# Kernel tuning notes

Measured on AMD Instinct MI355X. Metric: run time of the kernel, lower is better.

The kernel has to match this reference:

```python
import jax, jax.numpy as jnp
import numpy as np

LN_EPS = 1e-5

def layer_norm(h, gamma, beta):
    mu = jnp.mean(h, axis=-1, keepdims=True)
    var = jnp.mean(jnp.square(h - mu), axis=-1, keepdims=True)
    return (h - mu) * jax.lax.rsqrt(var + LN_EPS) * gamma + beta

def gcn_conv(x, src, dst, W, b, n_nodes):
    # PyG GCNConv: h = X W; out = D^-1/2 (A + I) D^-1/2 h + b
    h = x @ W
    deg = jax.ops.segment_sum(jnp.ones_like(src, dtype=h.dtype), dst, num_segments=n_nodes)
    dinv = jax.lax.rsqrt(jnp.maximum(deg, 1.0))  # deg >= 1 due to self-loops
    norm = dinv[src] * dinv[dst]                  # [E]
    msg = h[src] * norm[:, None]                  # [E, d]
    return jax.ops.segment_sum(msg, dst, num_segments=n_nodes) + b

def setup_inputs() -> dict:
    key = jax.random.key(0)
    ks = jax.random.split(key, 8)
    N, E, Cin, Ch, Cout = 10000, 160000, 256, 512, 256
    x = jax.random.normal(ks[0], (N, Cin), dtype=jnp.float32)
    edge_index = jax.random.randint(ks[1], (2, E), 0, N, dtype=jnp.int64)
    W1 = jax.random.normal(ks[2], (Cin, Ch), dtype=jnp.float32) * (1.0 / np.sqrt(Cin))
    b1 = jnp.zeros((Ch,), dtype=jnp.float32)
    gamma1 = jnp.ones((Ch,), dtype=jnp.float32)
    beta1 = jnp.zeros((Ch,), dtype=jnp.float32)
    W2 = jax.random.normal(ks[3], (Ch, Cout), dtype=jnp.float32) * (1.0 / np.sqrt(Ch))
    b2 = jnp.zeros((Cout,), dtype=jnp.float32)
    gamma2 = jnp.ones((Cout,), dtype=jnp.float32)
    beta2 = jnp.zeros((Cout,), dtype=jnp.float32)
    return {"x": x, "edge_index": edge_index, "W1": W1, "b1": b1,
            "gamma1": gamma1, "beta1": beta1, "W2": W2, "b2": b2,
            "gamma2": gamma2, "beta2": beta2}

def reference(x, edge_index, W1, b1, gamma1, beta1, W2, b2, gamma2, beta2):
    n = x.shape[0]
    loops = jnp.arange(n, dtype=edge_index.dtype)
    src = jnp.concatenate([edge_index[0], loops])
    dst = jnp.concatenate([edge_index[1], loops])
    h = gcn_conv(x, src, dst, W1, b1, n)
    h = jax.nn.relu(layer_norm(h, gamma1, beta1))  # dropout = identity (eval mode)
    g = gcn_conv(h, src, dst, W2, b2, n)
    g = jax.nn.relu(layer_norm(g, gamma2, beta2))
    return g
```

## Files before the change

### kernel.cpp

```cpp
#include <hip/hip_runtime.h>
#include <hip/hip_bf16.h>


typedef __attribute__((ext_vector_type(8))) short bf16x8;
typedef __attribute__((ext_vector_type(4))) float f32x4;
typedef __attribute__((ext_vector_type(4))) unsigned short us4;
typedef __attribute__((ext_vector_type(8))) unsigned short us8;

__device__ __forceinline__ unsigned short f2bf(float f) {
  unsigned int x = __float_as_uint(f);
  return (unsigned short)((x + 0x7FFFu + ((x >> 16) & 1u)) >> 16);
}
__device__ __forceinline__ float bf2f(unsigned short u) {
  return __uint_as_float((unsigned int)u << 16);
}

__device__ __forceinline__ void transpose_tile(const float* __restrict__ W,
                                               unsigned short* __restrict__ Wt,
                                               int K, int N, int n0, int k0,
                                               unsigned short (*t)[33], int tid) {
  int tx = tid & 31, ty = tid >> 5;
#pragma unroll
  for (int i = 0; i < 32; i += 8)
    t[ty + i][tx] = f2bf(W[(size_t)(k0 + ty + i) * N + n0 + tx]);
  __syncthreads();
#pragma unroll
  for (int i = 0; i < 32; i += 8)
    Wt[(size_t)(n0 + ty + i) * K + k0 + tx] = t[tx][ty + i];
}

__global__ __launch_bounds__(256) void prep_kernel(
    const float* __restrict__ x, unsigned short* __restrict__ xb, long nelem,
    const int* __restrict__ dst, int E, int* __restrict__ deg,
    const float* __restrict__ W1, unsigned short* __restrict__ W1t,
    const float* __restrict__ W2, unsigned short* __restrict__ W2t,
    int Cin, int Ch, int Cout, int nbx, int nbe, int nbw1) {
  __shared__ unsigned short t[32][33];
  int bid = blockIdx.x;
  int tid = threadIdx.x;
  if (bid < nbx) {
    long i = ((long)bid * 256 + tid) * 8;
    if (i + 8 <= nelem) {
      f32x4 a = *(const f32x4*)&x[i];
      f32x4 b = *(const f32x4*)&x[i + 4];
      us8 o;
      o[0] = f2bf(a.x); o[1] = f2bf(a.y); o[2] = f2bf(a.z); o[3] = f2bf(a.w);
      o[4] = f2bf(b.x); o[5] = f2bf(b.y); o[6] = f2bf(b.z); o[7] = f2bf(b.w);
      *(us8*)&xb[i] = o;
    }
  } else if (bid < nbx + nbe) {
    int e = (bid - nbx) * 256 + tid;
    if (e < E) atomicAdd(&deg[dst[e]], 1);
  } else if (bid < nbx + nbe + nbw1) {
    int ti = bid - nbx - nbe;
    int w1w = Ch >> 5;
    transpose_tile(W1, W1t, Cin, Ch, (ti % w1w) * 32, (ti / w1w) * 32, t, tid);
  } else {
    int ti = bid - nbx - nbe - nbw1;
    int w2w = Cout >> 5;
    transpose_tile(W2, W2t, Ch, Cout, (ti % w2w) * 32, (ti / w2w) * 32, t, tid);
  }
}

__global__ __launch_bounds__(1024) void scan_kernel(const int* __restrict__ deg, int N,
                                                    int* __restrict__ offsets,
                                                    int* __restrict__ curs,
                                                    float* __restrict__ dinv) {
  __shared__ int wsum[16];
  __shared__ int chunk_base;
  int tid = threadIdx.x;
  int lane = tid & 63, wid = tid >> 6;
  if (tid == 0) chunk_base = 0;
  __syncthreads();
  for (int c = 0; c < N; c += 1024) {
    int i = c + tid;
    int v = (i < N) ? deg[i] : 0;
    if (i < N) dinv[i] = rsqrtf((float)(v + 1));
    int s = v;
#pragma unroll
    for (int off = 1; off < 64; off <<= 1) {
      int t = __shfl_up(s, off, 64);
      if (lane >= off) s += t;
    }
    if (lane == 63) wsum[wid] = s;
    __syncthreads();
    if (wid == 0 && lane < 16) {
      int ws = wsum[lane];
      int t = ws;
#pragma unroll
      for (int off = 1; off < 16; off <<= 1) {
        int u = __shfl_up(t, off, 64);
        if (lane >= off) t += u;
      }
      wsum[lane] = t - ws;
    }
    __syncthreads();
    if (i < N) {
      int o = chunk_base + wsum[wid] + s - v;
      offsets[i] = o;
      curs[i] = o;
    }
    __syncthreads();
    if (tid == 1023) chunk_base += wsum[15] + s;
  }
  __syncthreads();
  if (tid == 0) offsets[N] = chunk_base;
}

__global__ __launch_bounds__(256) void fill_kernel(const int* __restrict__ src,
                                                   const int* __restrict__ dst, int E,
                                                   int* __restrict__ curs,
                                                   const float* __restrict__ dinv,
                                                   int* __restrict__ csr_src,
                                                   float* __restrict__ csr_norm) {
  int e = blockIdx.x * 256 + threadIdx.x;
  if (e >= E) return;
  int s = src[e], d = dst[e];
  int p = atomicAdd(&curs[d], 1);
  csr_src[p]  = s;
  csr_norm[p] = dinv[s] * dinv[d];
}


template <bool FUSE_LN, typename OutT>
__global__ __launch_bounds__(256) void agg_kernel(const unsigned short* __restrict__ H,
                                                  const int* __restrict__ csr_src,
                                                  const float* __restrict__ csr_norm,
                                                  const int* __restrict__ offsets,
                                                  const float* __restrict__ dinv,
                                                  const float* __restrict__ bias,
                                                  const float* __restrict__ gamma,
                                                  const float* __restrict__ beta,
                                                  OutT* __restrict__ out, int N) {
  int node = blockIdx.x * 4 + (threadIdx.x >> 6);
  if (node >= N) return;
  int lane = threadIdx.x & 63;
  int p0 = offsets[node], p1 = offsets[node + 1];
  f32x4 acc = {0.f, 0.f, 0.f, 0.f};
  for (int p = p0; p < p1; ++p) {
    int s    = csr_src[p];
    float wt = csr_norm[p];
    us4 hv = *(const us4*)&H[(size_t)s * 256 + lane * 4];
    acc.x = fmaf(bf2f(hv.x), wt, acc.x);
    acc.y = fmaf(bf2f(hv.y), wt, acc.y);
    acc.z = fmaf(bf2f(hv.z), wt, acc.z);
    acc.w = fmaf(bf2f(hv.w), wt, acc.w);
  }
  float dn = dinv[node];
  float w2 = dn * dn;
  us4 sv = *(const us4*)&H[(size_t)node * 256 + lane * 4];
  acc.x = fmaf(bf2f(sv.x), w2, acc.x);
  acc.y = fmaf(bf2f(sv.y), w2, acc.y);
  acc.z = fmaf(bf2f(sv.z), w2, acc.z);
  acc.w = fmaf(bf2f(sv.w), w2, acc.w);
  if (bias) acc += *(const f32x4*)&bias[lane * 4];
  if constexpr (FUSE_LN) {
    float s  = acc.x + acc.y + acc.z + acc.w;
    float ss = acc.x * acc.x + acc.y * acc.y + acc.z * acc.z + acc.w * acc.w;
#pragma unroll
    for (int off = 32; off > 0; off >>= 1) {
      s  += __shfl_xor(s, off, 64);
      ss += __shfl_xor(ss, off, 64);
    }
    float mu = s * (1.0f / 256.0f);
    float var = ss * (1.0f / 256.0f) - mu * mu;
    float r = rsqrtf(var + 1e-5f);
    f32x4 g  = *(const f32x4*)&gamma[lane * 4];
    f32x4 be = *(const f32x4*)&beta[lane * 4];
    f32x4 o;
    o.x = fmaxf((acc.x - mu) * r * g.x + be.x, 0.f);
    o.y = fmaxf((acc.y - mu) * r * g.y + be.y, 0.f);
    o.z = fmaxf((acc.z - mu) * r * g.z + be.z, 0.f);
    o.w = fmaxf((acc.w - mu) * r * g.w + be.w, 0.f);
    *(f32x4*)&out[(size_t)node * 256 + lane * 4] = o;
  } else {
    us4 o;
    o.x = f2bf(acc.x); o.y = f2bf(acc.y); o.z = f2bf(acc.z); o.w = f2bf(acc.w);
    *(us4*)&out[(size_t)node * 256 + lane * 4] = o;
  }
}


template <typename OutT>
__global__ __launch_bounds__(256) void mfma_gemm_kernel(
    const unsigned short* __restrict__ A, const unsigned short* __restrict__ Bt,
    const float* __restrict__ bias, OutT* __restrict__ C, int M, int K, int N) {
  __shared__ unsigned short As[64 * 32];
  __shared__ unsigned short Bs[128 * 32];
  int tid = threadIdx.x;
  int lane = tid & 63, wid = tid >> 6;
  int bm = blockIdx.x * 64, bn = blockIdx.y * 128;
  int wm = (wid >> 1) * 32, wn = (wid & 1) * 64;
  int srow = tid >> 2;
  int schunk = tid & 3;
  int frow = lane & 15, fk = lane >> 4;
  f32x4 acc[2][4] = {};

  for (int k0 = 0; k0 < K; k0 += 32) {
    {
      int row = srow;
      int scA = schunk ^ ((row >> 1) & 3);
      int ga = bm + row; ga = ga < M ? ga : M - 1;
      const unsigned short* gA = A + (size_t)ga * K + k0 + scA * 8;
      __builtin_amdgcn_global_load_lds(
          (const __attribute__((address_space(1))) unsigned int*)(const void*)gA,
          (__attribute__((address_space(3))) unsigned int*)(void*)(As + (wid * 16) * 32),
          16, 0, 0);
    }
#pragma unroll
    for (int r = 0; r < 2; ++r) {
      int row = r * 64 + srow;
      int scB = schunk ^ ((row >> 1) & 3);
      const unsigned short* gB = Bt + (size_t)(bn + row) * K + k0 + scB * 8;
      __builtin_amdgcn_global_load_lds(
          (const __attribute__((address_space(1))) unsigned int*)(const void*)gB,
          (__attribute__((address_space(3))) unsigned int*)(void*)(Bs + (r * 64 + wid * 16) * 32),
          16, 0, 0);
    }
    __syncthreads();
    bf16x8 af[2], bf[4];
#pragma unroll
    for (int mi = 0; mi < 2; ++mi) {
      int row = wm + mi * 16 + frow;
      int sc = fk ^ ((row >> 1) & 3);
      af[mi] = *(const bf16x8*)(As + row * 32 + sc * 8);
    }
#pragma unroll
    for (int ni = 0; ni < 4; ++ni) {
      int row = wn + ni * 16 + frow;
      int sc = fk ^ ((row >> 1) & 3);
      bf[ni] = *(const bf16x8*)(Bs + row * 32 + sc * 8);
    }
#pragma unroll
    for (int mi = 0; mi < 2; ++mi)
#pragma unroll
      for (int ni = 0; ni < 4; ++ni)
        acc[mi][ni] = __builtin_amdgcn_mfma_f32_16x16x32_bf16(af[mi], bf[ni], acc[mi][ni], 0, 0, 0);
    __syncthreads();
  }

  int row0 = bm + wm + fk * 4;
  int col0 = bn + wn + frow;
#pragma unroll
  for (int mi = 0; mi < 2; ++mi) {
#pragma unroll
    for (int ni = 0; ni < 4; ++ni) {
      int col = col0 + ni * 16;
      float bv = bias ? bias[col] : 0.0f;
#pragma unroll
      for (int r = 0; r < 4; ++r) {
        int row = row0 + mi * 16 + r;
        if (row < M) {
          float v = acc[mi][ni][r] + bv;
          if constexpr (sizeof(OutT) == 4) C[(size_t)row * N + col] = v;
          else                             C[(size_t)row * N + col] = f2bf(v);
        }
      }
    }
  }
}


__global__ __launch_bounds__(256) void ln_relu512_kernel(const float* __restrict__ in,
                                                         const float* __restrict__ gamma,
                                                         const float* __restrict__ beta,
                                                         unsigned short* __restrict__ out) {
  int row = blockIdx.x;
  const float* p = in + (size_t)row * 512;
  int tid = threadIdx.x;
  float v0 = p[tid];
  float v1 = p[tid + 256];
  float s = v0 + v1;
  float ss = v0 * v0 + v1 * v1;
#pragma unroll
  for (int off = 32; off > 0; off >>= 1) {
    s  += __shfl_down(s, off, 64);
    ss += __shfl_down(ss, off, 64);
  }
  __shared__ float sh[8];
  int wid = tid >> 6;
  if ((tid & 63) == 0) { sh[wid] = s; sh[4 + wid] = ss; }
  __syncthreads();
  s  = sh[0] + sh[1] + sh[2] + sh[3];
  ss = sh[4] + sh[5] + sh[6] + sh[7];
  float mu = s * (1.0f / 512.0f);
  float var = ss * (1.0f / 512.0f) - mu * mu;
  float r = rsqrtf(var + 1e-5f);
  out[(size_t)row * 512 + tid]       = f2bf(fmaxf((v0 - mu) * r * gamma[tid] + beta[tid], 0.0f));
  out[(size_t)row * 512 + tid + 256] = f2bf(fmaxf((v1 - mu) * r * gamma[tid + 256] + beta[tid + 256], 0.0f));
}


extern "C" void kernel_launch(void* const* d_in, const int* in_sizes, int n_in,
                              void* d_out, int out_size, void* d_ws, size_t ws_size,
                              hipStream_t stream) {
  const float* x    = (const float*)d_in[0];
  const int*   ei   = (const int*)d_in[1];
  const float* W1   = (const float*)d_in[2];
  const float* b1   = (const float*)d_in[3];
  const float* ga1  = (const float*)d_in[4];
  const float* be1  = (const float*)d_in[5];
  const float* W2   = (const float*)d_in[6];
  const float* b2   = (const float*)d_in[7];
  const float* ga2  = (const float*)d_in[8];
  const float* be2  = (const float*)d_in[9];
  float* out = (float*)d_out;

  const int Ch   = in_sizes[3];
  const int Cout = in_sizes[7];
  const int Cin  = in_sizes[2] / Ch;
  const int N    = in_sizes[0] / Cin;
  const int E    = in_sizes[1] / 2;
  const int* srcp = ei;
  const int* dstp = ei + E;

  char* ws = (char*)d_ws;
  size_t off = 0;
  auto alloc = [&](size_t bytes) -> void* {
    off = (off + 255) & ~(size_t)255;
    void* p = ws + off;
    off += bytes;
    return p;
  };
  unsigned short* xb   = (unsigned short*)alloc((size_t)N * Cin * 2);
  unsigned short* axb  = (unsigned short*)alloc((size_t)N * Cin * 2);
  float*          h1   = (float*)alloc((size_t)N * Ch * 4);
  unsigned short* h1b  = (unsigned short*)alloc((size_t)N * Ch * 2);
  unsigned short* h2b  = (unsigned short*)alloc((size_t)N * Cout * 2);
  unsigned short* W1t  = (unsigned short*)alloc((size_t)Cin * Ch * 2);
  unsigned short* W2t  = (unsigned short*)alloc((size_t)Ch * Cout * 2);
  int*   deg   = (int*)alloc((size_t)N * 4);
  int*   curs  = (int*)alloc((size_t)N * 4);
  int*   offs  = (int*)alloc((size_t)(N + 1) * 4);
  float* dinv  = (float*)alloc((size_t)N * 4);
  int*   csr_s = (int*)alloc((size_t)E * 4);
  float* csr_n = (float*)alloc((size_t)E * 4);

  hipMemsetAsync(deg, 0, (size_t)N * 4, stream);

  long nelem = (long)N * Cin;
  int nbx  = (int)((nelem / 8 + 255) / 256);
  int nbe  = (E + 255) / 256;
  int nbw1 = (Cin / 32) * (Ch / 32);
  int nbw2 = (Ch / 32) * (Cout / 32);
  prep_kernel<<<nbx + nbe + nbw1 + nbw2, 256, 0, stream>>>(
      x, xb, nelem, dstp, E, deg, W1, W1t, W2, W2t, Cin, Ch, Cout, nbx, nbe, nbw1);
  scan_kernel<<<1, 1024, 0, stream>>>(deg, N, offs, curs, dinv);
  fill_kernel<<<nbe, 256, 0, stream>>>(srcp, dstp, E, curs, dinv, csr_s, csr_n);

  agg_kernel<false, unsigned short><<<(N + 3) / 4, 256, 0, stream>>>(
      xb, csr_s, csr_n, offs, dinv, nullptr, nullptr, nullptr, axb, N);
  mfma_gemm_kernel<float><<<dim3((N + 63) / 64, Ch / 128), 256, 0, stream>>>(
      axb, W1t, b1, h1, N, Cin, Ch);
  ln_relu512_kernel<<<N, 256, 0, stream>>>(h1, ga1, be1, h1b);

  mfma_gemm_kernel<unsigned short><<<dim3((N + 63) / 64, Cout / 128), 256, 0, stream>>>(
      h1b, W2t, nullptr, h2b, N, Ch, Cout);
  agg_kernel<true, float><<<(N + 3) / 4, 256, 0, stream>>>(
      h2b, csr_s, csr_n, offs, dinv, b2, ga2, be2, out, N);
}
```

Baseline: 204.9 us.

## Pack CSR into int2, prefetch neighbor rows in aggregation, double-buffer GEMM LDS

The CSR source index and edge norm are now stored together as one int2, so each edge needs a single 8-byte load instead of two separate loads. The aggregation loop is software-pipelined: it fetches the next edge record and the next neighbor feature row before doing the FMAs for the current one, to hide gather latency. The MFMA GEMM moves to double-buffered LDS tiles and issues the next K-slice's global-to-LDS loads before computing on the current one. The extra barrier waits may still serialize the GEMM loads, and the doubled shared memory could lower occupancy.

Result: faster. 189.9 us (-7.3%).

```diff
diff --git a/kernel.cpp b/kernel.cpp
--- a/kernel.cpp
+++ b/kernel.cpp
@@ -27,6 +27,7 @@
 #pragma unroll
   for (int i = 0; i < 32; i += 8)
     Wt[(size_t)(n0 + ty + i) * K + k0 + tx] = t[tx][ty + i];
+  __syncthreads();
 }
 
 __global__ __launch_bounds__(256) void prep_kernel(
@@ -36,8 +37,7 @@
     const float* __restrict__ W2, unsigned short* __restrict__ W2t,
     int Cin, int Ch, int Cout, int nbx, int nbe, int nbw1) {
   __shared__ unsigned short t[32][33];
-  int bid = blockIdx.x;
-  int tid = threadIdx.x;
+  int bid = blockIdx.x, tid = threadIdx.x;
   if (bid < nbx) {
     long i = ((long)bid * 256 + tid) * 8;
     if (i + 8 <= nelem) {
@@ -53,12 +53,12 @@
     if (e < E) atomicAdd(&deg[dst[e]], 1);
   } else if (bid < nbx + nbe + nbw1) {
     int ti = bid - nbx - nbe;
-    int w1w = Ch >> 5;
-    transpose_tile(W1, W1t, Cin, Ch, (ti % w1w) * 32, (ti / w1w) * 32, t, tid);
+    int w = Ch >> 5;
+    transpose_tile(W1, W1t, Cin, Ch, (ti % w) * 32, (ti / w) * 32, t, tid);
   } else {
     int ti = bid - nbx - nbe - nbw1;
-    int w2w = Cout >> 5;
-    transpose_tile(W2, W2t, Ch, Cout, (ti % w2w) * 32, (ti / w2w) * 32, t, tid);
+    int w = Cout >> 5;
+    transpose_tile(W2, W2t, Ch, Cout, (ti % w) * 32, (ti / w) * 32, t, tid);
   }
 }
 
@@ -111,48 +111,55 @@
                                                    const int* __restrict__ dst, int E,
                                                    int* __restrict__ curs,
                                                    const float* __restrict__ dinv,
-                                                   int* __restrict__ csr_src,
-                                                   float* __restrict__ csr_norm) {
+                                                   int2* __restrict__ csr_sn) {
   int e = blockIdx.x * 256 + threadIdx.x;
   if (e >= E) return;
   int s = src[e], d = dst[e];
   int p = atomicAdd(&curs[d], 1);
-  csr_src[p]  = s;
-  csr_norm[p] = dinv[s] * dinv[d];
-}
-
+  csr_sn[p] = make_int2(s, __float_as_int(dinv[s] * dinv[d]));
+}
+
+
+#define AGG_FMA(hv, wt)                      \
+  acc.x = fmaf(bf2f((hv).x), (wt), acc.x);   \
+  acc.y = fmaf(bf2f((hv).y), (wt), acc.y);   \
+  acc.z = fmaf(bf2f((hv).z), (wt), acc.z);   \
+  acc.w = fmaf(bf2f((hv).w), (wt), acc.w);
 
 template <bool FUSE_LN, typename OutT>
-__global__ __launch_bounds__(256) void agg_kernel(const unsigned short* __restrict__ H,
-                                                  const int* __restrict__ csr_src,
-                                                  const float* __restrict__ csr_norm,
-                                                  const int* __restrict__ offsets,
-                                                  const float* __restrict__ dinv,
-                                                  const float* __restrict__ bias,
-                                                  const float* __restrict__ gamma,
-                                                  const float* __restrict__ beta,
-                                                  OutT* __restrict__ out, int N) {
-  int node = blockIdx.x * 4 + (threadIdx.x >> 6);
-  if (node >= N) return;
-  int lane = threadIdx.x & 63;
-  int p0 = offsets[node], p1 = offsets[node + 1];
+__device__ __forceinline__ void agg_node(int node, int lane,
+                                         const unsigned short* __restrict__ H,
+                                         const int2* __restrict__ csr,
+                                         const int* __restrict__ offs,
+                                         const float* __restrict__ dinv,
+                                         const float* __restrict__ bias,
+                                         const float* __restrict__ gamma,
+                                         const float* __restrict__ beta,
+                                         OutT* __restrict__ out) {
+  int p0 = offs[node], p1 = offs[node + 1];
+  int n = p1 - p0;
   f32x4 acc = {0.f, 0.f, 0.f, 0.f};
-  for (int p = p0; p < p1; ++p) {
-    int s    = csr_src[p];
-    float wt = csr_norm[p];
-    us4 hv = *(const us4*)&H[(size_t)s * 256 + lane * 4];
-    acc.x = fmaf(bf2f(hv.x), wt, acc.x);
-    acc.y = fmaf(bf2f(hv.y), wt, acc.y);
-    acc.z = fmaf(bf2f(hv.z), wt, acc.z);
-    acc.w = fmaf(bf2f(hv.w), wt, acc.w);
+  if (n > 0) {
+    int2 e0 = csr[p0];
+    us4 h0 = *(const us4*)&H[(size_t)e0.x * 256 + lane * 4];
+    if (n > 1) {
+      int2 e1 = csr[p0 + 1];
+      for (int p = p0; p + 2 < p1; ++p) {
+        us4 h1v = *(const us4*)&H[(size_t)e1.x * 256 + lane * 4];
+        int2 e2 = csr[p + 2];
+        AGG_FMA(h0, __int_as_float(e0.y));
+        e0 = e1; h0 = h1v; e1 = e2;
+      }
+      us4 h1v = *(const us4*)&H[(size_t)e1.x * 256 + lane * 4];
+      AGG_FMA(h0, __int_as_float(e0.y));
+      AGG_FMA(h1v, __int_as_float(e1.y));
+    } else {
+      AGG_FMA(h0, __int_as_float(e0.y));
+    }
   }
   float dn = dinv[node];
-  float w2 = dn * dn;
   us4 sv = *(const us4*)&H[(size_t)node * 256 + lane * 4];
-  acc.x = fmaf(bf2f(sv.x), w2, acc.x);
-  acc.y = fmaf(bf2f(sv.y), w2, acc.y);
-  acc.z = fmaf(bf2f(sv.z), w2, acc.z);
-  acc.w = fmaf(bf2f(sv.w), w2, acc.w);
+  AGG_FMA(sv, dn * dn);
   if (bias) acc += *(const f32x4*)&bias[lane * 4];
   if constexpr (FUSE_LN) {
     float s  = acc.x + acc.y + acc.z + acc.w;
@@ -180,13 +187,27 @@
   }
 }
 
+template <bool FUSE_LN, typename OutT>
+__global__ __launch_bounds__(256) void agg_kernel(const unsigned short* __restrict__ H,
+                                                  const int2* __restrict__ csr,
+                                                  const int* __restrict__ offs,
+                                                  const float* __restrict__ dinv,
+                                                  const float* __restrict__ bias,
+                                                  const float* __restrict__ gamma,
+                                                  const float* __restrict__ beta,
+                                                  OutT* __restrict__ out, int N) {
+  int node = blockIdx.x * 4 + (threadIdx.x >> 6);
+  if (node >= N) return;
+  agg_node<FUSE_LN, OutT>(node, threadIdx.x & 63, H, csr, offs, dinv, bias, gamma, beta, out);
+}
+
 
 template <typename OutT>
 __global__ __launch_bounds__(256) void mfma_gemm_kernel(
     const unsigned short* __restrict__ A, const unsigned short* __restrict__ Bt,
     const float* __restrict__ bias, OutT* __restrict__ C, int M, int K, int N) {
-  __shared__ unsigned short As[64 * 32];
-  __shared__ unsigned short Bs[128 * 32];
+  __shared__ unsigned short As[2][64 * 32];
+  __shared__ unsigned short Bs[2][128 * 32];
   int tid = threadIdx.x;
   int lane = tid & 63, wid = tid >> 6;
   int bm = blockIdx.x * 64, bn = blockIdx.y * 128;
@@ -196,40 +217,49 @@
   int frow = lane & 15, fk = lane >> 4;
   f32x4 acc[2][4] = {};
 
-  for (int k0 = 0; k0 < K; k0 += 32) {
-    {
-      int row = srow;
-      int scA = schunk ^ ((row >> 1) & 3);
-      int ga = bm + row; ga = ga < M ? ga : M - 1;
-      const unsigned short* gA = A + (size_t)ga * K + k0 + scA * 8;
-      __builtin_amdgcn_global_load_lds(
-          (const __attribute__((address_space(1))) unsigned int*)(const void*)gA,
-          (__attribute__((address_space(3))) unsigned int*)(void*)(As + (wid * 16) * 32),
-          16, 0, 0);
-    }
-#pragma unroll
-    for (int r = 0; r < 2; ++r) {
-      int row = r * 64 + srow;
-      int scB = schunk ^ ((row >> 1) & 3);
-      const unsigned short* gB = Bt + (size_t)(bn + row) * K + k0 + scB * 8;
-      __builtin_amdgcn_global_load_lds(
-          (const __attribute__((address_space(1))) unsigned int*)(const void*)gB,
-          (__attribute__((address_space(3))) unsigned int*)(void*)(Bs + (r * 64 + wid * 16) * 32),
-          16, 0, 0);
-    }
-    __syncthreads();
+  int scA = schunk ^ ((srow >> 1) & 3);
+  int gaA = bm + srow; gaA = gaA < M ? gaA : M - 1;
+  const unsigned short* gA0 = A + (size_t)gaA * K + scA * 8;
+  int rowB0 = srow, rowB1 = 64 + srow;
+  int scB0 = schunk ^ ((rowB0 >> 1) & 3);
+  int scB1 = schunk ^ ((rowB1 >> 1) & 3);
+  const unsigned short* gB0 = Bt + (size_t)(bn + rowB0) * K + scB0 * 8;
+  const unsigned short* gB1 = Bt + (size_t)(bn + rowB1) * K + scB1 * 8;
+
+  auto stage = [&](int k0, unsigned short* Ad, unsigned short* Bd) {
+    __builtin_amdgcn_global_load_lds(
+        (const __attribute__((address_space(1))) unsigned int*)(const void*)(gA0 + k0),
+        (__attribute__((address_space(3))) unsigned int*)(void*)(Ad + (wid * 16) * 32),
+        16, 0, 0);
+    __builtin_amdgcn_global_load_lds(
+        (const __attribute__((address_space(1))) unsigned int*)(const void*)(gB0 + k0),
+        (__attribute__((address_space(3))) unsigned int*)(void*)(Bd + (wid * 16) * 32),
+        16, 0, 0);
+    __builtin_amdgcn_global_load_lds(
+        (const __attribute__((address_space(1))) unsigned int*)(const void*)(gB1 + k0),
+        (__attribute__((address_space(3))) unsigned int*)(void*)(Bd + (64 + wid * 16) * 32),
+        16, 0, 0);
+  };
+
+  int nk = K >> 5;
+  stage(0, As[0], Bs[0]);
+  __syncthreads();
+  for (int k = 0; k < nk; ++k) {
+    unsigned short* Ac = As[k & 1];
+    unsigned short* Bc = Bs[k & 1];
+    if (k + 1 < nk) stage((k + 1) << 5, As[(k + 1) & 1], Bs[(k + 1) & 1]);
     bf16x8 af[2], bf[4];
 #pragma unroll
     for (int mi = 0; mi < 2; ++mi) {
       int row = wm + mi * 16 + frow;
       int sc = fk ^ ((row >> 1) & 3);
-      af[mi] = *(const bf16x8*)(As + row * 32 + sc * 8);
+      af[mi] = *(const bf16x8*)(Ac + row * 32 + sc * 8);
     }
 #pragma unroll
     for (int ni = 0; ni < 4; ++ni) {
       int row = wn + ni * 16 + frow;
       int sc = fk ^ ((row >> 1) & 3);
-      bf[ni] = *(const bf16x8*)(Bs + row * 32 + sc * 8);
+      bf[ni] = *(const bf16x8*)(Bc + row * 32 + sc * 8);
     }
 #pragma unroll
     for (int mi = 0; mi < 2; ++mi)
@@ -333,8 +363,7 @@
   int*   curs  = (int*)alloc((size_t)N * 4);
   int*   offs  = (int*)alloc((size_t)(N + 1) * 4);
   float* dinv  = (float*)alloc((size_t)N * 4);
-  int*   csr_s = (int*)alloc((size_t)E * 4);
-  float* csr_n = (float*)alloc((size_t)E * 4);
+  int2*  csr   = (int2*)alloc((size_t)E * 8);
 
   hipMemsetAsync(deg, 0, (size_t)N * 4, stream);
 
@@ -346,10 +375,10 @@
   prep_kernel<<<nbx + nbe + nbw1 + nbw2, 256, 0, stream>>>(
       x, xb, nelem, dstp, E, deg, W1, W1t, W2, W2t, Cin, Ch, Cout, nbx, nbe, nbw1);
   scan_kernel<<<1, 1024, 0, stream>>>(deg, N, offs, curs, dinv);
-  fill_kernel<<<nbe, 256, 0, stream>>>(srcp, dstp, E, curs, dinv, csr_s, csr_n);
+  fill_kernel<<<nbe, 256, 0, stream>>>(srcp, dstp, E, curs, dinv, csr);
 
   agg_kernel<false, unsigned short><<<(N + 3) / 4, 256, 0, stream>>>(
-      xb, csr_s, csr_n, offs, dinv, nullptr, nullptr, nullptr, axb, N);
+      xb, csr, offs, dinv, nullptr, nullptr, nullptr, axb, N);
   mfma_gemm_kernel<float><<<dim3((N + 63) / 64, Ch / 128), 256, 0, stream>>>(
       axb, W1t, b1, h1, N, Cin, Ch);
   ln_relu512_kernel<<<N, 256, 0, stream>>>(h1, ga1, be1, h1b);
@@ -357,5 +386,5 @@
   mfma_gemm_kernel<unsigned short><<<dim3((N + 63) / 64, Cout / 128), 256, 0, stream>>>(
       h1b, W2t, nullptr, h2b, N, Ch, Cout);
   agg_kernel<true, float><<<(N + 3) / 4, 256, 0, stream>>>(
-      h2b, csr_s, csr_n, offs, dinv, b2, ga2, be2, out, N);
-}
+      h2b, csr, offs, dinv, b2, ga2, be2, out, N);
+}
```
